# Kernel tuning notes

Measured on AMD Instinct MI355X. Metric: run time of the kernel, lower is better.

## Reference

```python
import jax, jax.numpy as jnp
import numpy as np

N = 16384          # batch of signals
DIM_T = 256        # time steps per signal
DT = 0.01          # integration dt (intg_lev=1 -> dt_intg = dt)
NUF = 256          # num_units_feat
HID_XI = 128       # hidlayers_xi
HID_AUX = 64       # hidlayers_aux1_dec
LEN_INTG = DIM_T   # (dim_t-1)*intg_lev + 1 with intg_lev=1


def _linear_init(key, fan_in, fan_out):
    # torch nn.Linear default: U(-1/sqrt(fan_in), 1/sqrt(fan_in))
    s = 1.0 / np.sqrt(fan_in)
    kw, kb = jax.random.split(key)
    W = jax.random.uniform(kw, (fan_in, fan_out), minval=-s, maxval=s, dtype=jnp.float32)
    b = jax.random.uniform(kb, (fan_out,), minval=-s, maxval=s, dtype=jnp.float32)
    return W, b


def setup_inputs() -> dict:
    key = jax.random.key(0)
    ks = jax.random.split(key, 12)
    data = jax.random.normal(ks[0], (N, DIM_T), dtype=jnp.float32)
    omega = jax.random.normal(ks[1], (N, 1), dtype=jnp.float32)
    eps = jax.random.normal(ks[2], (N, 1), dtype=jnp.float32)
    # feature extractor (mlp branch): [dim_t+1 -> 256 -> 256], relu after both (actfun_output=True)
    W_feat1, b_feat1 = _linear_init(ks[3], DIM_T + 1, NUF)
    W_feat2, b_feat2 = _linear_init(ks[4], NUF, NUF)
    # xi mean head: MLP [256 -> 128 -> 1] then Softplus
    W_xim1, b_xim1 = _linear_init(ks[5], NUF, HID_XI)
    W_xim2, b_xim2 = _linear_init(ks[6], HID_XI, 1)
    # xi lnvar head: MLP [256 -> 128 -> 1]
    W_xil1, b_xil1 = _linear_init(ks[7], NUF, HID_XI)
    W_xil2, b_xil2 = _linear_init(ks[8], HID_XI, 1)
    # decoder aux1 MLP: [dim_z_aux1+1=2 -> 64 -> 1]
    W_aux1, b_aux1 = _linear_init(ks[9], 2, HID_AUX)
    W_aux2, b_aux2 = _linear_init(ks[10], HID_AUX, 1)
    return dict(data=data, omega=omega, eps=eps,
                W_feat1=W_feat1, b_feat1=b_feat1, W_feat2=W_feat2, b_feat2=b_feat2,
                W_xim1=W_xim1, b_xim1=b_xim1, W_xim2=W_xim2, b_xim2=b_xim2,
                W_xil1=W_xil1, b_xil1=b_xil1, W_xil2=W_xil2, b_xil2=b_xil2,
                W_aux1=W_aux1, b_aux1=b_aux1, W_aux2=W_aux2, b_aux2=b_aux2)


def reference(data, omega, eps,
              W_feat1, b_feat1, W_feat2, b_feat2,
              W_xim1, b_xim1, W_xim2, b_xim2,
              W_xil1, b_xil1, W_xil2, b_xil2,
              W_aux1, b_aux1, W_aux2, b_aux2):
    relu = jax.nn.relu
    # ---- encode_xi ----
    x_ = jnp.concatenate([data, omega], axis=1)                 # [n, dim_t+1]
    feat = relu(relu(x_ @ W_feat1 + b_feat1) @ W_feat2 + b_feat2)  # [n, 256]
    xi_mean = jax.nn.softplus(relu(feat @ W_xim1 + b_xim1) @ W_xim2 + b_xim2)  # [n, 1]
    xi_lnvar = relu(feat @ W_xil1 + b_xil1) @ W_xil2 + b_xil2                  # [n, 1]
    # ---- draw (reparameterization + clamp to feasible range [0, 1]) ----
    xi = xi_mean + jnp.exp(0.5 * xi_lnvar) * eps
    xi = jnp.clip(xi, 0.0, 1.0)
    # ---- decode: Euler odeint over LEN_INTG steps of state yy=[y, dy/dt] ----
    init_y = data[:, :1]                                        # [n, 1]
    initcond = jnp.concatenate([init_y, jnp.zeros_like(init_y)], axis=1)  # [n, 2]

    def step(yy, _):
        # physics: d[y, v]/dt = [v, 0]; aux MLP adds acceleration from (z_aux1=omega, y)
        aux_in = jnp.concatenate([omega, yy[:, :1]], axis=1)    # [n, 2]
        acc = relu(aux_in @ W_aux1 + b_aux1) @ W_aux2 + b_aux2  # [n, 1]
        dyy = jnp.concatenate([yy[:, 1:2], acc], axis=1)        # [n, 2]
        return yy + DT * dyy, yy

    _, yy_seq = jax.lax.scan(step, initcond, None, length=LEN_INTG)  # [len_intg, n, 2]
    y_seq = yy_seq[:, :, 0].T                                   # [n, dim_t] (intg_lev=1)
    t_intg = DT * jnp.arange(LEN_INTG, dtype=jnp.float32)       # [dim_t]
    x_PAB = jnp.exp(-jnp.abs(xi) * t_intg[None, :]) * y_seq     # [n, dim_t]
    return xi_mean, xi_lnvar, x_PAB
```

## Files before the change

kernel.cpp:

```cpp
#include <hip/hip_runtime.h>
#include <math.h>

#define NROWS 16384
#define DT_C 0.01f

typedef short s16x8 __attribute__((ext_vector_type(8)));
typedef float f32x4 __attribute__((ext_vector_type(4)));
typedef float f32x2 __attribute__((ext_vector_type(2)));

__device__ __forceinline__ unsigned short f2bf(float f) {
    unsigned u = __float_as_uint(f);
    u += 0x7fffu + ((u >> 16) & 1u);
    return (unsigned short)(u >> 16);
}
__device__ __forceinline__ unsigned pack2bf(float a, float b) {
    return (unsigned)f2bf(a) | ((unsigned)f2bf(b) << 16);
}
template <int CTRL>
__device__ __forceinline__ float dppadd(float v) {
    int x = __builtin_amdgcn_update_dpp(0, __float_as_int(v), CTRL, 0xF, 0xF, true);
    return v + __int_as_float(x);
}
__device__ __forceinline__ float sum4(float p) {
    p = dppadd<0xB1>(p);
    p = dppadd<0x4E>(p);
    return p;
}
__device__ __forceinline__ float sum8(float p) {
    p = dppadd<0xB1>(p);
    p = dppadd<0x4E>(p);
    p = dppadd<0x141>(p);
    return p;
}

__global__ __launch_bounds__(256) void prep_k(
    const float* __restrict__ Wf1, const float* __restrict__ Wf2,
    const float* __restrict__ Wm1, const float* __restrict__ Wl1,
    const float* __restrict__ bm1, const float* __restrict__ bl1,
    unsigned short* __restrict__ wpack, float* __restrict__ biasH)
{
    const int id = blockIdx.x * 256 + threadIdx.x;
    const int n  = id & 255;
    const int k8 = (id >> 8) & 31;
    const int s  = id >> 13;

    unsigned short tmp[8];
    #pragma unroll
    for (int j = 0; j < 8; ++j) {
        const int k = k8 * 8 + j;
        float v;
        if (s == 0)      v = Wf1[k * 256 + n];
        else if (s == 1) v = Wf2[k * 256 + n];
        else             v = (n < 128) ? Wm1[k * 128 + n] : Wl1[k * 128 + n - 128];
        tmp[j] = f2bf(v);
    }
    *(uint4*)&wpack[((s * 32 + k8) * 256 + n) * 8] = *(const uint4*)tmp;

    if (id < 256) biasH[id] = (id < 128) ? bm1[id] : bl1[id - 128];
}

__global__ __launch_bounds__(512, 2) void fused_k(
    const float* __restrict__ data, const float* __restrict__ omega,
    const float* __restrict__ eps_g,
    const unsigned short* __restrict__ wpack, const float* __restrict__ biasH,
    const float* __restrict__ bf1, const float* __restrict__ bf2,
    const float* __restrict__ w256g,
    const float* __restrict__ Wm2, const float* __restrict__ bm2,
    const float* __restrict__ Wl2, const float* __restrict__ bl2,
    const float* __restrict__ Wa1, const float* __restrict__ ba1,
    const float* __restrict__ Wa2, const float* __restrict__ ba2,
    float* __restrict__ out_mean, float* __restrict__ out_lnvar,
    float* __restrict__ xout)
{
    __shared__ __align__(16) unsigned char smem[66048];
    unsigned short* As1 = (unsigned short*)smem;
    unsigned short* Hs  = (unsigned short*)(smem + 32768);
    float* headsF = (float*)smem;
    float* omg = (float*)(smem + 65536);
    float* xiS = (float*)(smem + 65792);

    const int tid  = threadIdx.x;
    const int wid  = tid >> 6;
    const int lane = tid & 63;
    const int ln   = lane & 15;
    const int quad = lane >> 4;
    const int r0   = blockIdx.x * 64;

    {
        #pragma unroll
        for (int g2 = 0; g2 < 8; ++g2) {
            const int unit = g2 * 512 + tid;
            const int m    = unit >> 6;
            const int c16  = unit & 63;
            const int kblk = c16 >> 1;
            const int h    = c16 & 1;
            const float4 v = *(const float4*)&data[(size_t)(r0 + m) * 256 + c16 * 4];
            unsigned* d = (unsigned*)&As1[((kblk * 64) + (m ^ (kblk & 7))) * 8 + h * 4];
            d[0] = pack2bf(v.x, v.y);
            d[1] = pack2bf(v.z, v.w);
        }
        if (tid < 64) omg[tid] = omega[r0 + tid];
    }
    __syncthreads();

    f32x4 acc[4][2];

    auto seed = [&](const float* bias) {
        #pragma unroll
        for (int nt = 0; nt < 2; ++nt) {
            const float b = bias[wid * 32 + nt * 16 + ln];
            #pragma unroll
            for (int mt = 0; mt < 4; ++mt) acc[mt][nt] = f32x4{b, b, b, b};
        }
    };

    auto run_stage = [&](const unsigned short* Ap, const unsigned short* wp) {
        #pragma unroll
        for (int c = 0; c < 4; ++c) {
            #pragma unroll
            for (int kk = 0; kk < 2; ++kk) {
                const int kb   = kk * 4 + quad;
                const int kblk = c * 8 + kb;
                const int f    = kblk & 7;
                s16x8 b0 = *(const s16x8*)&wp[((size_t)(kblk * 256) + wid * 32 + 0 * 16 + ln) * 8];
                s16x8 b1 = *(const s16x8*)&wp[((size_t)(kblk * 256) + wid * 32 + 1 * 16 + ln) * 8];
                #pragma unroll
                for (int mt = 0; mt < 4; ++mt) {
                    s16x8 a = *(const s16x8*)&Ap[((size_t)kblk * 64 + ((ln ^ f) + 16 * mt)) * 8];
                    acc[mt][0] = __builtin_amdgcn_mfma_f32_16x16x32_bf16(a, b0, acc[mt][0], 0, 0, 0);
                    acc[mt][1] = __builtin_amdgcn_mfma_f32_16x16x32_bf16(a, b1, acc[mt][1], 0, 0, 0);
                }
            }
        }
    };

    auto write_packed = [&](unsigned short* dst, bool addOm) {
        #pragma unroll
        for (int nt = 0; nt < 2; ++nt) {
            const int col = wid * 32 + nt * 16 + ln;
            const int kg  = col >> 3, f = kg & 7, jj = col & 7;
            const float wo = addOm ? w256g[col] : 0.f;
            #pragma unroll
            for (int mt = 0; mt < 4; ++mt) {
                #pragma unroll
                for (int r = 0; r < 4; ++r) {
                    const int row = mt * 16 + quad * 4 + r;
                    float v = acc[mt][nt][r];
                    if (addOm) v = fmaf(omg[row], wo, v);
                    v = fmaxf(v, 0.f);
                    dst[(kg * 64 + (row ^ f)) * 8 + jj] = f2bf(v);
                }
            }
        }
    };

    seed(bf1);
    run_stage(As1, wpack);
    write_packed(Hs, true);
    __syncthreads();
    seed(bf2);
    run_stage(Hs, wpack + 65536);
    write_packed(As1, false);
    __syncthreads();
    seed(biasH);
    run_stage(As1, wpack + 131072);
    __syncthreads();
    #pragma unroll
    for (int nt = 0; nt < 2; ++nt) {
        const int col = wid * 32 + nt * 16 + ln;
        #pragma unroll
        for (int mt = 0; mt < 4; ++mt) {
            #pragma unroll
            for (int r = 0; r < 4; ++r) {
                const int row = mt * 16 + quad * 4 + r;
                headsF[row * 256 + ((col + row * 8) & 255)] = fmaxf(acc[mt][nt][r], 0.f);
            }
        }
    }
    __syncthreads();

    {
        const int m = tid >> 3, l = tid & 7;
        float pm = 0.f, pl = 0.f;
        #pragma unroll
        for (int q = 0; q < 4; ++q) {
            const int c0 = l * 16 + q * 4;
            const float4 hm = *(const float4*)&headsF[m * 256 + ((c0 + m * 8) & 255)];
            const float4 wm = *(const float4*)&Wm2[c0];
            const float4 hl = *(const float4*)&headsF[m * 256 + ((128 + c0 + m * 8) & 255)];
            const float4 wl = *(const float4*)&Wl2[c0];
            pm = fmaf(hm.w, wm.w, fmaf(hm.z, wm.z, fmaf(hm.y, wm.y, fmaf(hm.x, wm.x, pm))));
            pl = fmaf(hl.w, wl.w, fmaf(hl.z, wl.z, fmaf(hl.y, wl.y, fmaf(hl.x, wl.x, pl))));
        }
        pm = sum8(pm);
        pl = sum8(pl);
        if (l == 0) {
            const float xm  = pm + bm2[0];
            const float mean = fmaxf(xm, 0.f) + log1pf(expf(-fabsf(xm)));
            const float lnv  = pl + bl2[0];
            out_mean[r0 + m]  = mean;
            out_lnvar[r0 + m] = lnv;
            float xi = mean + expf(0.5f * lnv) * eps_g[r0 + m];
            xiS[m] = fminf(fmaxf(xi, 0.f), 1.f);
        }
    }
    __syncthreads();

    if (tid >= 256) return;

    {
        const int r   = tid >> 2;
        const int l   = tid & 3;
        const int row = r0 + r;
        const float om = omg[r];
        const float pseed = ba2[0] * 0.25f;

        f32x2 w1v[8], Av[8], w2v[8];
        #pragma unroll
        for (int i = 0; i < 8; ++i) {
            const f32x2 w0 = *(const f32x2*)&Wa1[l * 16 + i * 2];
            const f32x2 bb = *(const f32x2*)&ba1[l * 16 + i * 2];
            w1v[i] = *(const f32x2*)&Wa1[64 + l * 16 + i * 2];
            w2v[i] = *(const f32x2*)&Wa2[l * 16 + i * 2];
            Av[i]  = f32x2{fmaf(om, w0.x, bb.x), fmaf(om, w0.y, bb.y)};
        }

        auto partial = [&](float y) -> float {
            const f32x2 y2 = f32x2{y, y};
            f32x2 aA = f32x2{pseed, 0.f};
            f32x2 aB = f32x2{0.f, 0.f};
            #pragma unroll
            for (int i = 0; i < 4; ++i) {
                f32x2 h = __builtin_elementwise_fma(y2, w1v[i], Av[i]);
                h = __builtin_elementwise_max(h, f32x2{0.f, 0.f});
                aA = __builtin_elementwise_fma(h, w2v[i], aA);
            }
            #pragma unroll
            for (int i = 4; i < 8; ++i) {
                f32x2 g = __builtin_elementwise_fma(y2, w1v[i], Av[i]);
                g = __builtin_elementwise_max(g, f32x2{0.f, 0.f});
                aB = __builtin_elementwise_fma(g, w2v[i], aB);
            }
            return (aA.x + aA.y) + (aB.x + aB.y);
        };

        const float xi   = xiS[r];
        const float dfac = expf(-xi * DT_C);
        const float y0   = data[(size_t)row * 256];
        float ym = y0;
        float yc = y0;
        float d  = 1.f;
        const float DT2 = DT_C * DT_C;
        float pr = sum4(partial(ym));

        float* orow = xout + (size_t)row * 256 + l * 4;
        for (int tb = 0; tb < 16; ++tb) {
            float cur[4];
            #pragma unroll
            for (int j = 0; j < 16; ++j) {
                if ((j >> 2) == l) cur[j & 3] = ym * d;
                float pn = sum4(partial(yc));
                const float ynext = fmaf(DT2, pr, fmaf(2.f, yc, -ym));
                ym = yc; yc = ynext; pr = pn;
                d *= dfac;
            }
            *(float4*)&orow[tb * 16] = *(const float4*)cur;
        }
    }
}

extern "C" void kernel_launch(void* const* d_in, const int* in_sizes, int n_in,
                              void* d_out, int out_size, void* d_ws, size_t ws_size,
                              hipStream_t stream)
{
    const float* data    = (const float*)d_in[0];
    const float* omega   = (const float*)d_in[1];
    const float* eps     = (const float*)d_in[2];
    const float* W_feat1 = (const float*)d_in[3];
    const float* b_feat1 = (const float*)d_in[4];
    const float* W_feat2 = (const float*)d_in[5];
    const float* b_feat2 = (const float*)d_in[6];
    const float* W_xim1  = (const float*)d_in[7];
    const float* b_xim1  = (const float*)d_in[8];
    const float* W_xim2  = (const float*)d_in[9];
    const float* b_xim2  = (const float*)d_in[10];
    const float* W_xil1  = (const float*)d_in[11];
    const float* b_xil1  = (const float*)d_in[12];
    const float* W_xil2  = (const float*)d_in[13];
    const float* b_xil2  = (const float*)d_in[14];
    const float* W_aux1  = (const float*)d_in[15];
    const float* b_aux1  = (const float*)d_in[16];
    const float* W_aux2  = (const float*)d_in[17];
    const float* b_aux2  = (const float*)d_in[18];

    float* out_mean  = (float*)d_out;
    float* out_lnvar = out_mean + NROWS;
    float* out_x     = out_lnvar + NROWS;

    unsigned short* wpack = (unsigned short*)d_ws;
    float* biasH = (float*)((char*)d_ws + 3 * 32 * 256 * 8 * 2);

    prep_k<<<96, 256, 0, stream>>>(W_feat1, W_feat2, W_xim1, W_xil1,
                                   b_xim1, b_xil1, wpack, biasH);
    fused_k<<<256, 512, 0, stream>>>(data, omega, eps, wpack, biasH,
                                     b_feat1, b_feat2, W_feat1 + 256 * 256,
                                     W_xim2, b_xim2, W_xil2, b_xil2,
                                     W_aux1, b_aux1, W_aux2, b_aux2,
                                     out_mean, out_lnvar, out_x);
}
```

Measured before the change: 137.4 us.

## Split ODE aux MLP across 8 lanes and interleave two rows per lane group

The Euler integration phase now gives each group of 8 lanes two rows instead of one row per group of 4 lanes. Each lane evaluates 8 hidden units per row, and the two independent row recurrences are interleaved to hide the DPP reduction and FMA dependency latency. The cost is a third DPP step (sum8 instead of sum4) per timestep and more live registers for the two row states.

```diff
diff --git a/kernel.cpp b/kernel.cpp
--- a/kernel.cpp
+++ b/kernel.cpp
@@ -20,11 +20,6 @@
 __device__ __forceinline__ float dppadd(float v) {
     int x = __builtin_amdgcn_update_dpp(0, __float_as_int(v), CTRL, 0xF, 0xF, true);
     return v + __int_as_float(x);
-}
-__device__ __forceinline__ float sum4(float p) {
-    p = dppadd<0xB1>(p);
-    p = dppadd<0x4E>(p);
-    return p;
 }
 __device__ __forceinline__ float sum8(float p) {
     p = dppadd<0xB1>(p);
@@ -209,62 +204,69 @@
     if (tid >= 256) return;
 
     {
-        const int r   = tid >> 2;
-        const int l   = tid & 3;
-        const int row = r0 + r;
-        const float om = omg[r];
-        const float pseed = ba2[0] * 0.25f;
-
-        f32x2 w1v[8], Av[8], w2v[8];
-        #pragma unroll
-        for (int i = 0; i < 8; ++i) {
-            const f32x2 w0 = *(const f32x2*)&Wa1[l * 16 + i * 2];
-            const f32x2 bb = *(const f32x2*)&ba1[l * 16 + i * 2];
-            w1v[i] = *(const f32x2*)&Wa1[64 + l * 16 + i * 2];
-            w2v[i] = *(const f32x2*)&Wa2[l * 16 + i * 2];
-            Av[i]  = f32x2{fmaf(om, w0.x, bb.x), fmaf(om, w0.y, bb.y)};
-        }
-
-        auto partial = [&](float y) -> float {
+        const int w  = tid >> 6;
+        const int g  = (tid & 63) >> 3;
+        const int l  = tid & 7;
+        const int rA = w * 16 + g;
+        const int rB = w * 16 + 8 + g;
+        const float omA = omg[rA];
+        const float omB = omg[rB];
+        const float pseed = ba2[0] * 0.125f;
+
+        f32x2 w1v[4], w2v[4], AvA[4], AvB[4];
+        #pragma unroll
+        for (int i = 0; i < 4; ++i) {
+            const f32x2 w0 = *(const f32x2*)&Wa1[l * 8 + i * 2];
+            const f32x2 bb = *(const f32x2*)&ba1[l * 8 + i * 2];
+            w1v[i] = *(const f32x2*)&Wa1[64 + l * 8 + i * 2];
+            w2v[i] = *(const f32x2*)&Wa2[l * 8 + i * 2];
+            AvA[i] = f32x2{fmaf(omA, w0.x, bb.x), fmaf(omA, w0.y, bb.y)};
+            AvB[i] = f32x2{fmaf(omB, w0.x, bb.x), fmaf(omB, w0.y, bb.y)};
+        }
+
+        auto partial = [&](float y, const f32x2* Av) -> float {
             const f32x2 y2 = f32x2{y, y};
-            f32x2 aA = f32x2{pseed, 0.f};
-            f32x2 aB = f32x2{0.f, 0.f};
+            f32x2 acc2 = f32x2{pseed, 0.f};
             #pragma unroll
             for (int i = 0; i < 4; ++i) {
                 f32x2 h = __builtin_elementwise_fma(y2, w1v[i], Av[i]);
                 h = __builtin_elementwise_max(h, f32x2{0.f, 0.f});
-                aA = __builtin_elementwise_fma(h, w2v[i], aA);
-            }
-            #pragma unroll
-            for (int i = 4; i < 8; ++i) {
-                f32x2 g = __builtin_elementwise_fma(y2, w1v[i], Av[i]);
-                g = __builtin_elementwise_max(g, f32x2{0.f, 0.f});
-                aB = __builtin_elementwise_fma(g, w2v[i], aB);
-            }
-            return (aA.x + aA.y) + (aB.x + aB.y);
+                acc2 = __builtin_elementwise_fma(h, w2v[i], acc2);
+            }
+            return acc2.x + acc2.y;
         };
 
-        const float xi   = xiS[r];
-        const float dfac = expf(-xi * DT_C);
-        const float y0   = data[(size_t)row * 256];
-        float ym = y0;
-        float yc = y0;
-        float d  = 1.f;
         const float DT2 = DT_C * DT_C;
-        float pr = sum4(partial(ym));
-
-        float* orow = xout + (size_t)row * 256 + l * 4;
-        for (int tb = 0; tb < 16; ++tb) {
-            float cur[4];
-            #pragma unroll
-            for (int j = 0; j < 16; ++j) {
-                if ((j >> 2) == l) cur[j & 3] = ym * d;
-                float pn = sum4(partial(yc));
-                const float ynext = fmaf(DT2, pr, fmaf(2.f, yc, -ym));
-                ym = yc; yc = ynext; pr = pn;
-                d *= dfac;
-            }
-            *(float4*)&orow[tb * 16] = *(const float4*)cur;
+        const float dfacA = expf(-xiS[rA] * DT_C);
+        const float dfacB = expf(-xiS[rB] * DT_C);
+        const float y0A = data[(size_t)(r0 + rA) * 256];
+        const float y0B = data[(size_t)(r0 + rB) * 256];
+        float ymA = y0A, ycA = y0A, dA = 1.f;
+        float ymB = y0B, ycB = y0B, dB = 1.f;
+        float prA = sum8(partial(ymA, AvA));
+        float prB = sum8(partial(ymB, AvB));
+
+        float* orowA = xout + (size_t)(r0 + rA) * 256 + l * 4;
+        float* orowB = xout + (size_t)(r0 + rB) * 256 + l * 4;
+        for (int tb = 0; tb < 8; ++tb) {
+            float curA[4], curB[4];
+            #pragma unroll
+            for (int j = 0; j < 32; ++j) {
+                if ((j >> 2) == l) {
+                    curA[j & 3] = ymA * dA;
+                    curB[j & 3] = ymB * dB;
+                }
+                float pnA = partial(ycA, AvA);
+                float pnB = partial(ycB, AvB);
+                pnA = sum8(pnA);
+                pnB = sum8(pnB);
+                const float ynA = fmaf(DT2, prA, fmaf(2.f, ycA, -ymA));
+                const float ynB = fmaf(DT2, prB, fmaf(2.f, ycB, -ymB));
+                ymA = ycA; ycA = ynA; prA = pnA; dA *= dfacA;
+                ymB = ycB; ycB = ynB; prB = pnB; dB *= dfacB;
+            }
+            *(float4*)&orowA[tb * 32] = *(const float4*)curA;
+            *(float4*)&orowB[tb * 32] = *(const float4*)curB;
         }
     }
 }
```

New measurement: 142.8 us. +3.9%, slower.
